# Optimization experiments

Hardware: AMD Instinct MI355X
Metric: run time of the kernel (lower is better)

## Reference

```python
import jax, jax.numpy as jnp
import numpy as np

K = 32  # kneighbors
BN_EPS = 1e-5


def setup_inputs() -> dict:
    key = jax.random.key(0)
    ks = jax.random.split(key, 8)
    B, N, S, C = 8, 4096, 1024, 64
    Cin = C + 6  # 70
    inp = {
        "xyz": jax.random.normal(ks[0], (B, N, 3), jnp.float32),
        "points": jax.random.normal(ks[1], (B, C, N), jnp.float32),
        "new_xyz": jax.random.normal(ks[2], (B, S, 3), jnp.float32),
        "W1": jax.random.normal(ks[3], (128, Cin), jnp.float32) / np.sqrt(Cin),
        "b1": jax.random.normal(ks[4], (128,), jnp.float32) * 0.01,
        "g1": jnp.ones((128,), jnp.float32),
        "be1": jnp.zeros((128,), jnp.float32),
        "W2": jax.random.normal(ks[5], (256, 128), jnp.float32) / np.sqrt(128),
        "b2": jax.random.normal(ks[6], (256,), jnp.float32) * 0.01,
        "g2": jnp.ones((256,), jnp.float32),
        "be2": jnp.zeros((256,), jnp.float32),
    }
    return inp


def _forward(xyz, points, new_xyz, W1, b1, g1, be1, W2, b2, g2, be2):
    B, S, _ = new_xyz.shape
    pts = jnp.transpose(points, (0, 2, 1))  # [B,N,C]
    # squared pairwise distances [B,S,N]
    sqd = (jnp.sum(new_xyz ** 2, -1)[:, :, None]
           + jnp.sum(xyz ** 2, -1)[:, None, :]
           - 2.0 * jnp.einsum('bsc,bnc->bsn', new_xyz, xyz))
    _, idx = jax.lax.top_k(-sqd, K)  # k smallest -> [B,S,K] int32
    gather = jax.vmap(lambda a, i: a[i])  # per-batch fancy gather
    gxyz = gather(xyz, idx)   # [B,S,K,3]
    gpts = gather(pts, idx)   # [B,S,K,C]
    q = jnp.broadcast_to(new_xyz[:, :, None, :], (B, S, K, 3))
    g = jnp.concatenate([gpts, gxyz, q], axis=-1)  # [B,S,K,C+6]
    x = jnp.transpose(g, (0, 3, 2, 1))  # [B,Cin,K,S]
    for W, b, gm, bt in ((W1, b1, g1, be1), (W2, b2, g2, be2)):
        x = jnp.einsum('oi,biks->boks', W, x) + b[None, :, None, None]
        mu = jnp.mean(x, axis=(0, 2, 3), keepdims=True)
        var = jnp.var(x, axis=(0, 2, 3), keepdims=True)  # biased, as torch BN train
        x = (x - mu) * jax.lax.rsqrt(var + BN_EPS)
        x = x * gm[None, :, None, None] + bt[None, :, None, None]
        x = jax.nn.relu(x)
    new_points = jnp.max(x, axis=2)  # [B,Cout,S]
    return new_xyz, new_points


def reference(xyz, points, new_xyz, W1, b1, g1, be1, W2, b2, g2, be2):
    return _forward(xyz, points, new_xyz, W1, b1, g1, be1, W2, b2, g2, be2)
```

## Files before the change

kernel.cpp:

```cpp
#include <hip/hip_runtime.h>
#include <stdint.h>

constexpr int Bn = 8, Nn = 4096, Sn = 1024, Cc = 64, KNN = 32, C1 = 128, C2 = 256;
constexpr int Qq = Bn * Sn;
constexpr int Mm = Qq * KNN;
constexpr int OUT_XYZ = Bn * Sn * 3;
constexpr float BNEPS = 1e-5f;
constexpr unsigned RSEL = 9;

constexpr size_t SZ_IDX  = (size_t)Qq * KNN * 4;
constexpr size_t SZ_PTST = (size_t)Bn * Nn * Cc * 2;
constexpr int    NB_MLP  = Mm / 64;
constexpr size_t SZ_P1   = (size_t)NB_MLP * 256 * 4;
constexpr size_t SZ_P2   = (size_t)NB_MLP * 512 * 4;
constexpr size_t OFF_IDX  = 0;
constexpr size_t OFF_PTST = OFF_IDX + SZ_IDX;
constexpr size_t OFF_P1   = OFF_PTST + SZ_PTST;
constexpr size_t OFF_P2   = OFF_P1 + SZ_P1;
constexpr size_t OFF_P1B  = OFF_P2 + SZ_P2;
constexpr size_t OFF_P2B  = OFF_P1B + (size_t)128 * 256 * 4;
constexpr size_t OFF_BN1  = OFF_P2B + (size_t)128 * 512 * 4;
constexpr size_t OFF_W2F  = OFF_BN1 + 1024;
constexpr size_t OFF_W1F  = OFF_W2F + (size_t)32768 * 2;
constexpr size_t OFF_VAL  = (OFF_W1F + (size_t)12288 * 2 + 255) & ~(size_t)255;

typedef __attribute__((ext_vector_type(8))) __bf16 bf16x8;
typedef __attribute__((ext_vector_type(4))) float f32x4;

__device__ __forceinline__ unsigned short f2bf(float f) {
  unsigned u = __float_as_uint(f);
  u = u + 0x7FFFu + ((u >> 16) & 1u);
  return (unsigned short)(u >> 16);
}

__device__ __forceinline__ void agg_hist(unsigned* hist, unsigned bin, bool valid, int lane) {
  bool todo = valid;
  while (true) {
    unsigned long long bm = __ballot(todo);
    if (bm == 0ull) break;
    int first = __ffsll(bm) - 1;
    unsigned b = (unsigned)__shfl((int)bin, first);
    unsigned long long m = __ballot(todo && bin == b);
    if (lane == first) atomicAdd(&hist[b], (unsigned)__popcll(m));
    if (todo && bin == b) todo = false;
  }
}

__global__ __launch_bounds__(256) void k_knn(const float* __restrict__ xyz,
                                             const float* __restrict__ nxyz,
                                             int* __restrict__ idxout,
                                             const float* __restrict__ pts,
                                             const float* __restrict__ W1,
                                             const float* __restrict__ W2,
                                             unsigned short* __restrict__ ptsTbf,
                                             float* __restrict__ outdst,
                                             unsigned short* __restrict__ w1f,
                                             unsigned short* __restrict__ w2f) {
  int t = threadIdx.x;
  if (blockIdx.x >= (unsigned)Qq) {
    int blk = blockIdx.x - Qq;
    if (blk < 512) {
      __shared__ float tile[64][65];
      int b = blk >> 6, n0 = (blk & 63) * 64;
      int cl = t & 63, rw = t >> 6;
#pragma unroll
      for (int i = 0; i < 16; ++i) {
        int c = i * 4 + rw;
        tile[cl][c] = pts[((size_t)b * Cc + c) * Nn + n0 + cl];
      }
      __syncthreads();
#pragma unroll
      for (int i = 0; i < 16; ++i) {
        int nf = i * 4 + rw;
        ptsTbf[((size_t)b * Nn + n0 + nf) * Cc + cl] = f2bf(tile[nf][cl]);
      }
    } else if (blk < 608) {
      int i = t + (blk - 512) * 256;
      if (i < OUT_XYZ) outdst[i] = nxyz[i];
    } else if (blk < 656) {
      int u = t + (blk - 608) * 256;
      int j = u & 7, lane = (u >> 3) & 63, rest = u >> 9;
      int ks = rest % 3, nt = rest / 3;
      int ch = nt * 16 + (lane & 15);
      int k = ks * 32 + (lane >> 4) * 8 + j;
      w1f[u] = (k < 70) ? f2bf(W1[ch * 70 + k]) : (unsigned short)0;
    } else {
      int u = t + (blk - 656) * 256;
      int j = u & 7, lane = (u >> 3) & 63, ks = (u >> 9) & 3, ntile = u >> 11;
      int col = ntile * 16 + (lane & 15);
      int k = ks * 32 + (lane >> 4) * 8 + j;
      w2f[u] = f2bf(W2[col * C1 + k]);
    }
    return;
  }
  int q = blockIdx.x, b = q >> 10;
  int lane = t & 63, w = t >> 6;
  const float4* xb4 = reinterpret_cast<const float4*>(xyz + (size_t)b * Nn * 3);
  float qx = nxyz[q * 3 + 0], qy = nxyz[q * 3 + 1], qz = nxyz[q * 3 + 2];
  unsigned key[16];
  {
#pragma clang fp contract(off)
    float sqq = (qx * qx + qy * qy) + qz * qz;
#pragma unroll
    for (int h = 0; h < 2; ++h) {
      float fl[24];
#pragma unroll
      for (int j = 0; j < 6; ++j) {
        float4 v = xb4[t * 12 + h * 6 + j];
        fl[4 * j + 0] = v.x; fl[4 * j + 1] = v.y; fl[4 * j + 2] = v.z; fl[4 * j + 3] = v.w;
      }
#pragma unroll
      for (int i = 0; i < 8; ++i) {
        float xl = fl[3 * i], yl = fl[3 * i + 1], zl = fl[3 * i + 2];
        float sqp = (xl * xl + yl * yl) + zl * zl;
        float dot = __builtin_fmaf(qz, zl, __builtin_fmaf(qy, yl, qx * xl));
        float d = (sqq + sqp) - 2.0f * dot;
        unsigned u = __float_as_uint(d);
        key[h * 8 + i] = (u & 0x80000000u) ? ~u : (u | 0x80000000u);
      }
    }
  }
  __shared__ unsigned long long buf64[256];
  __shared__ unsigned hist[256];
  __shared__ unsigned hist2[256];
  __shared__ unsigned wsum[4];
  __shared__ unsigned sel_bin, sel_off, cnt, ovf, thrU, tieflag;
  __shared__ unsigned eqcnt;
  __shared__ int eqbuf[128];

  unsigned s0 = key[0], s1 = key[8];
  hist[t] = 0;
  hist2[t] = 0;
  if (t == 0) { cnt = 0; ovf = 0; thrU = 0xFFFFFFFFu; tieflag = 0; }
  __syncthreads();
  agg_hist(hist, s0 >> 24, true, lane);
  agg_hist(hist, s1 >> 24, true, lane);
  __syncthreads();
  {
    unsigned h = hist[t], v = h;
#pragma unroll
    for (int off = 1; off < 64; off <<= 1) {
      unsigned o = __shfl_up(v, off);
      if (lane >= off) v += o;
    }
    if (lane == 63) wsum[w] = v;
    __syncthreads();
    unsigned woff = 0;
    for (int ww = 0; ww < w; ++ww) woff += wsum[ww];
    v += woff;
    unsigned vex = v - h;
    if (vex < RSEL && RSEL <= v) { sel_bin = (unsigned)t; sel_off = RSEL - vex; }
    __syncthreads();
  }
  unsigned sbin = sel_bin, srem = sel_off;
  if ((s0 >> 24) == sbin) atomicAdd(&hist2[(s0 >> 16) & 255u], 1u);
  if ((s1 >> 24) == sbin) atomicAdd(&hist2[(s1 >> 16) & 255u], 1u);
  __syncthreads();
  {
    unsigned h = hist2[t], v = h;
#pragma unroll
    for (int off = 1; off < 64; off <<= 1) {
      unsigned o = __shfl_up(v, off);
      if (lane >= off) v += o;
    }
    if (lane == 63) wsum[w] = v;
    __syncthreads();
    unsigned woff = 0;
    for (int ww = 0; ww < w; ++ww) woff += wsum[ww];
    v += woff;
    unsigned vex = v - h;
    if (vex < srem && srem <= v) {
      unsigned p16 = (sbin << 8) | (unsigned)t;
      thrU = (p16 >= 0xFFFFu) ? 0xFFFFFFFFu : ((p16 + 1u) << 16);
    }
    __syncthreads();
  }
  unsigned U = thrU;
#pragma unroll
  for (int i = 0; i < 16; ++i) {
    bool take = key[i] < U;
    unsigned long long m = __ballot(take);
    if (m == 0ull) continue;
    unsigned base = 0;
    if (lane == 0) base = atomicAdd(&cnt, (unsigned)__popcll(m));
    base = (unsigned)__shfl((int)base, 0);
    if (take) {
      unsigned off = base + (unsigned)__popcll(m & ((1ull << lane) - 1ull));
      if (off < 256u)
        buf64[off] = ((unsigned long long)key[i] << 32) | (unsigned)(t * 16 + i);
      else
        ovf = 1;
    }
  }
  __syncthreads();
  unsigned ncnt = cnt;
  if (!ovf && ncnt >= (unsigned)KNN && ncnt <= 256u) {
    int nc = (int)ncnt;
    const unsigned* keyhw = reinterpret_cast<const unsigned*>(buf64);
    int r = 0;
    bool own = false;
    int cid = 0;
    if (nc <= 64) {
      unsigned mykey = (lane < nc) ? keyhw[2 * lane + 1] : 0xFFFFFFFFu;
      int partial = 0;
      int base = w * 16;
#pragma unroll
      for (int ii = 0; ii < 16; ++ii) {
        int i = base + ii;
        bool inr = (i < nc);
        unsigned ok = (unsigned)__builtin_amdgcn_readlane((int)mykey, i);
        partial += (inr && ok < mykey);
      }
      hist[w * 64 + lane] = (unsigned)partial;
      __syncthreads();
      if (t < 64) {
        r = (int)(hist[t] + hist[64 + t] + hist[128 + t] + hist[192 + t]);
        cid = t;
        own = (t < nc);
      }
    } else if (nc <= 128) {
      cid = t & 127;
      bool haveC = (cid < nc);
      unsigned mykey = haveC ? keyhw[2 * cid + 1] : 0xFFFFFFFFu;
      int partial = 0;
      int c = t >> 7;
      if (c * 64 < nc) {
        int ci = c * 64 + lane;
        unsigned bk = (ci < nc) ? keyhw[2 * ci + 1] : 0xFFFFFFFFu;
#pragma unroll
        for (int i = 0; i < 64; ++i) {
          unsigned ok = (unsigned)__builtin_amdgcn_readlane((int)bk, i);
          partial += (ok < mykey);
        }
      }
      hist[t] = (unsigned)partial;
      __syncthreads();
      if (t < 128) {
        r = (int)(hist[t] + hist[t + 128]);
        own = haveC;
      }
    } else {
      cid = t;
      bool haveC = (t < nc);
      unsigned mykey = haveC ? keyhw[2 * t + 1] : 0xFFFFFFFFu;
      int nchunk = (nc + 63) >> 6;
      for (int c = 0; c < nchunk; ++c) {
        int ci = c * 64 + lane;
        unsigned bk = (ci < nc) ? keyhw[2 * ci + 1] : 0xFFFFFFFFu;
#pragma unroll
        for (int i = 0; i < 64; ++i) {
          unsigned ok = (unsigned)__builtin_amdgcn_readlane((int)bk, i);
          r += (ok < mykey);
        }
      }
      own = haveC;
    }
    hist2[t] = 0;
    __syncthreads();
    if (own) atomicAdd(&hist2[r], 1u);
    __syncthreads();
    if (hist2[t] > 1u) tieflag = 1;
    __syncthreads();
    if (tieflag) {
      bool own2 = (t < nc);
      unsigned long long my64 = own2 ? buf64[t] : ~0ull;
      int rr = 0;
      int nchunk = (nc + 63) >> 6;
      for (int c = 0; c < nchunk; ++c) {
        int ci = c * 64 + lane;
        unsigned long long v = (ci < nc) ? buf64[ci] : ~0ull;
        unsigned vlo = (unsigned)v, vhi = (unsigned)(v >> 32);
#pragma unroll
        for (int i = 0; i < 64; ++i) {
          unsigned olo = (unsigned)__builtin_amdgcn_readlane((int)vlo, i);
          unsigned ohi = (unsigned)__builtin_amdgcn_readlane((int)vhi, i);
          unsigned long long o = ((unsigned long long)ohi << 32) | olo;
          rr += (o < my64);
        }
      }
      if (own2 && rr < KNN) idxout[q * KNN + rr] = (int)keyhw[2 * t];
    } else {
      if (own && r < KNN) idxout[q * KNN + r] = (int)keyhw[2 * cid];
    }
  } else {
    unsigned prefix = 0, remaining = (unsigned)KNN;
    if (t == 0) { cnt = 0; eqcnt = 0; }
#pragma unroll
    for (int shift = 24; shift >= 0; shift -= 8) {
      hist[t] = 0;
      __syncthreads();
      unsigned himask = (shift == 24) ? 0u : (0xFFFFFFFFu << ((shift + 8) & 31));
#pragma unroll
      for (int i = 0; i < 16; ++i)
        if ((key[i] & himask) == prefix)
          atomicAdd(&hist[(key[i] >> shift) & 255], 1u);
      __syncthreads();
      unsigned h = hist[t], v = h;
#pragma unroll
      for (int off = 1; off < 64; off <<= 1) {
        unsigned o = __shfl_up(v, off);
        if (lane >= off) v += o;
      }
      if (lane == 63) wsum[w] = v;
      __syncthreads();
      unsigned woff = 0;
      for (int ww = 0; ww < w; ++ww) woff += wsum[ww];
      v += woff;
      unsigned vex = v - h;
      if (vex < remaining && remaining <= v) { sel_bin = (unsigned)t; sel_off = vex; }
      __syncthreads();
      prefix |= sel_bin << shift;
      remaining -= sel_off;
    }
#pragma unroll
    for (int i = 0; i < 16; ++i) {
      int p = t * 16 + i;
      if (key[i] < prefix) {
        unsigned pos = atomicAdd(&cnt, 1u);
        idxout[q * KNN + pos] = p;
      } else if (key[i] == prefix) {
        unsigned e = atomicAdd(&eqcnt, 1u);
        if (e < 128u) eqbuf[e] = p;
      }
    }
    __syncthreads();
    if (t == 0) {
      int n = (int)min(eqcnt, 128u);
      for (int a = 1; a < n; ++a) {
        int x = eqbuf[a], bi = a - 1;
        while (bi >= 0 && eqbuf[bi] > x) { eqbuf[bi + 1] = eqbuf[bi]; --bi; }
        eqbuf[bi + 1] = x;
      }
      int base = (int)cnt;
      for (int j = 0; j < (int)remaining; ++j) idxout[q * KNN + base + j] = eqbuf[j];
    }
  }
}

__device__ __forceinline__ void stage_gather(unsigned short* zs,
                                             const unsigned short* __restrict__ ptsTbf,
                                             const float* __restrict__ xyz,
                                             const float* __restrict__ nxyz,
                                             const int* __restrict__ idx,
                                             int m0, int b, int t) {
  int j = t >> 2, part = t & 3;
  int m = m0 + j;
  int pid = idx[m];
  const uint4* src =
      reinterpret_cast<const uint4*>(ptsTbf + ((size_t)b * Nn + pid) * Cc + part * 16);
  char* zc = reinterpret_cast<char*>(zs);
  int base = j * 256, swz = (j & 7) << 4;
  uint4 s0 = src[0], s1 = src[1];
  *reinterpret_cast<uint4*>(zc + ((base + part * 32) ^ swz)) = s0;
  *reinterpret_cast<uint4*>(zc + ((base + part * 32 + 16) ^ swz)) = s1;
  uint4 ex = make_uint4(0u, 0u, 0u, 0u);
  if (part == 0) {
    const float* xp = xyz + ((size_t)b * Nn + pid) * 3;
    int s = (m >> 5) & (Sn - 1);
    const float* qp = nxyz + (size_t)(b * Sn + s) * 3;
    ex.x = (unsigned)f2bf(xp[0]) | ((unsigned)f2bf(xp[1]) << 16);
    ex.y = (unsigned)f2bf(xp[2]) | ((unsigned)f2bf(qp[0]) << 16);
    ex.z = (unsigned)f2bf(qp[1]) | ((unsigned)f2bf(qp[2]) << 16);
  }
  *reinterpret_cast<uint4*>(zc + ((base + (8 + part) * 16) ^ swz)) = ex;
}

__global__ __launch_bounds__(256) void k_mlp1s(const unsigned short* __restrict__ ptsTbf,
                                               const float* __restrict__ xyz,
                                               const float* __restrict__ nxyz,
                                               const int* __restrict__ idx,
                                               const unsigned short* __restrict__ w1f,
                                               const float* __restrict__ b1,
                                               float* __restrict__ part1) {
  __shared__ unsigned short zs[64 * 128];
  int t = threadIdx.x;
  int m0 = blockIdx.x * 64;
  int b = m0 >> 15;
  int lane = t & 63, w = t >> 6;
  bf16x8 bfrag[2][3];
  {
    const uint4* wp = reinterpret_cast<const uint4*>(w1f);
#pragma unroll
    for (int nt = 0; nt < 2; ++nt)
#pragma unroll
      for (int ks = 0; ks < 3; ++ks)
        bfrag[nt][ks] = __builtin_bit_cast(bf16x8, wp[((w * 2 + nt) * 3 + ks) * 64 + lane]);
  }
  stage_gather(zs, ptsTbf, xyz, nxyz, idx, m0, b, t);
  __syncthreads();
  f32x4 acc[4][2];
#pragma unroll
  for (int mt = 0; mt < 4; ++mt)
#pragma unroll
    for (int nt = 0; nt < 2; ++nt) acc[mt][nt] = f32x4{0.f, 0.f, 0.f, 0.f};
  int r15 = lane & 15, rhi = lane >> 4;
  const char* zc = reinterpret_cast<const char*>(zs);
#pragma unroll
  for (int mt = 0; mt < 4; ++mt) {
    int row = mt * 16 + r15;
    bf16x8 af[3];
#pragma unroll
    for (int ks = 0; ks < 3; ++ks)
      af[ks] = __builtin_bit_cast(
          bf16x8, *reinterpret_cast<const uint4*>(
                      zc + ((row * 256 + ks * 64 + rhi * 16) ^ ((row & 7) << 4))));
#pragma unroll
    for (int nt = 0; nt < 2; ++nt)
#pragma unroll
      for (int ks = 0; ks < 3; ++ks)
        acc[mt][nt] =
            __builtin_amdgcn_mfma_f32_16x16x32_bf16(af[ks], bfrag[nt][ks], acc[mt][nt], 0, 0, 0);
  }
#pragma unroll
  for (int nt = 0; nt < 2; ++nt) {
    int col = w * 32 + nt * 16 + r15;
    float bv = b1[col];
    float s = 0.f, ss = 0.f;
#pragma unroll
    for (int mt = 0; mt < 4; ++mt)
#pragma unroll
      for (int rg = 0; rg < 4; ++rg) {
        float v = acc[mt][nt][rg] + bv;
        s += v; ss += v * v;
      }
    s += __shfl_xor(s, 16); s += __shfl_xor(s, 32);
    ss += __shfl_xor(ss, 16); ss += __shfl_xor(ss, 32);
    if (lane < 16) {
      part1[(size_t)blockIdx.x * 256 + col] = s;
      part1[(size_t)blockIdx.x * 256 + 128 + col] = ss;
    }
  }
}

__global__ __launch_bounds__(256) void k_red1a(const float* __restrict__ part1,
                                               float* __restrict__ p1b) {
  int t = threadIdx.x, r = blockIdx.x;
  float acc = 0.f;
  for (int row = r * 32; row < r * 32 + 32; ++row)
    acc += part1[(size_t)row * 256 + t];
  p1b[r * 256 + t] = acc;
}
__global__ __launch_bounds__(256) void k_red1b(const float* __restrict__ p1b,
                                               const float* __restrict__ b1,
                                               const float* __restrict__ g1,
                                               const float* __restrict__ be1,
                                               float* __restrict__ bn1) {
  __shared__ float lds[256];
  int t = threadIdx.x;
  float acc = 0.f;
  for (int row = 0; row < 128; ++row) acc += p1b[row * 256 + t];
  lds[t] = acc;
  __syncthreads();
  if (t < 128) {
    float sum = lds[t], ss = lds[128 + t];
    float mean = sum / (float)Mm;
    float var = ss / (float)Mm - mean * mean;
    float a = g1[t] * rsqrtf(var + BNEPS);
    bn1[t] = a;
    bn1[128 + t] = a * b1[t] + (be1[t] - mean * a);
  }
}

__global__ __launch_bounds__(256) void k_m2f(const unsigned short* __restrict__ ptsTbf,
                                             const float* __restrict__ xyz,
                                             const float* __restrict__ nxyz,
                                             const int* __restrict__ idx,
                                             const unsigned short* __restrict__ w1f,
                                             const float* __restrict__ bn1c,
                                             const unsigned short* __restrict__ w2f,
                                             const float* __restrict__ b2,
                                             const float* __restrict__ g2,
                                             float* __restrict__ part2,
                                             float* __restrict__ valv) {
  __shared__ unsigned short zs[64 * 128];
  __shared__ float bns[256];
  int t = threadIdx.x;
  int m0 = blockIdx.x * 64;
  int b = m0 >> 15;
  int lane = t & 63, w = t >> 6;
  bns[t] = bn1c[t];
  bf16x8 b1frag[2][3];
  {
    const uint4* wp = reinterpret_cast<const uint4*>(w1f);
#pragma unroll
    for (int nt = 0; nt < 2; ++nt)
#pragma unroll
      for (int ks = 0; ks < 3; ++ks)
        b1frag[nt][ks] = __builtin_bit_cast(bf16x8, wp[((w * 2 + nt) * 3 + ks) * 64 + lane]);
  }
  stage_gather(zs, ptsTbf, xyz, nxyz, idx, m0, b, t);
  __syncthreads();
  int r15 = lane & 15, rhi = lane >> 4;
  f32x4 acc1[4][2];
#pragma unroll
  for (int mt = 0; mt < 4; ++mt)
#pragma unroll
    for (int nt = 0; nt < 2; ++nt) acc1[mt][nt] = f32x4{0.f, 0.f, 0.f, 0.f};
  {
    const char* zc = reinterpret_cast<const char*>(zs);
#pragma unroll
    for (int mt = 0; mt < 4; ++mt) {
      int row = mt * 16 + r15;
      bf16x8 af[3];
#pragma unroll
      for (int ks = 0; ks < 3; ++ks)
        af[ks] = __builtin_bit_cast(
            bf16x8, *reinterpret_cast<const uint4*>(
                        zc + ((row * 256 + ks * 64 + rhi * 16) ^ ((row & 7) << 4))));
#pragma unroll
      for (int nt = 0; nt < 2; ++nt)
#pragma unroll
        for (int ks = 0; ks < 3; ++ks)
          acc1[mt][nt] = __builtin_amdgcn_mfma_f32_16x16x32_bf16(af[ks], b1frag[nt][ks],
                                                                 acc1[mt][nt], 0, 0, 0);
    }
  }
  __syncthreads();
  {
    char* zcw = reinterpret_cast<char*>(zs);
#pragma unroll
    for (int nt = 0; nt < 2; ++nt) {
      int col = w * 32 + nt * 16 + r15;
      float a = bns[col], c = bns[128 + col];
#pragma unroll
      for (int mt = 0; mt < 4; ++mt)
#pragma unroll
        for (int rg = 0; rg < 4; ++rg) {
          int row = mt * 16 + rhi * 4 + rg;
          float z = fmaxf(0.f, a * acc1[mt][nt][rg] + c);
          *reinterpret_cast<unsigned short*>(
              zcw + ((row * 256 + col * 2) ^ ((row & 7) << 4))) = f2bf(z);
        }
    }
  }
  __syncthreads();
  bf16x8 b2frag[4][4];
  {
    const uint4* wp = reinterpret_cast<const uint4*>(w2f) + (size_t)(w * 4) * 4 * 64 + lane;
#pragma unroll
    for (int nt = 0; nt < 4; ++nt)
#pragma unroll
      for (int ks = 0; ks < 4; ++ks)
        b2frag[nt][ks] = __builtin_bit_cast(bf16x8, wp[(nt * 4 + ks) * 64]);
  }
  f32x4 acc[4][4];
#pragma unroll
  for (int mt = 0; mt < 4; ++mt)
#pragma unroll
    for (int nt = 0; nt < 4; ++nt) acc[mt][nt] = f32x4{0.f, 0.f, 0.f, 0.f};
  {
    const char* zc = reinterpret_cast<const char*>(zs);
#pragma unroll
    for (int mt = 0; mt < 4; ++mt) {
      int row = mt * 16 + r15;
      bf16x8 af[4];
#pragma unroll
      for (int ks = 0; ks < 4; ++ks)
        af[ks] = __builtin_bit_cast(
            bf16x8, *reinterpret_cast<const uint4*>(
                        zc + ((row * 256 + ks * 64 + rhi * 16) ^ ((row & 7) << 4))));
#pragma unroll
      for (int nt = 0; nt < 4; ++nt)
#pragma unroll
        for (int ks = 0; ks < 4; ++ks)
          acc[mt][nt] = __builtin_amdgcn_mfma_f32_16x16x32_bf16(af[ks], b2frag[nt][ks],
                                                                acc[mt][nt], 0, 0, 0);
    }
  }
  int wn0 = w * 64;
  int q0 = m0 >> 5;
#pragma unroll
  for (int nt = 0; nt < 4; ++nt) {
    int col = wn0 + nt * 16 + r15;
    float bv = b2[col];
    bool pos = (g2[col] >= 0.0f);
    float s = 0.f, ss = 0.f;
    float mA = -3.0e38f, mB = -3.0e38f, nA = 3.0e38f, nB = 3.0e38f;
#pragma unroll
    for (int mt = 0; mt < 4; ++mt)
#pragma unroll
      for (int rg = 0; rg < 4; ++rg) {
        float v = acc[mt][nt][rg] + bv;
        s += v; ss += v * v;
        if (mt < 2) { mA = fmaxf(mA, v); nA = fminf(nA, v); }
        else        { mB = fmaxf(mB, v); nB = fminf(nB, v); }
      }
    float vA = pos ? mA : nA, vB = pos ? mB : nB;
    s += __shfl_xor(s, 16); s += __shfl_xor(s, 32);
    ss += __shfl_xor(ss, 16); ss += __shfl_xor(ss, 32);
    if (pos) {
      vA = fmaxf(vA, __shfl_xor(vA, 16)); vA = fmaxf(vA, __shfl_xor(vA, 32));
      vB = fmaxf(vB, __shfl_xor(vB, 16)); vB = fmaxf(vB, __shfl_xor(vB, 32));
    } else {
      vA = fminf(vA, __shfl_xor(vA, 16)); vA = fminf(vA, __shfl_xor(vA, 32));
      vB = fminf(vB, __shfl_xor(vB, 16)); vB = fminf(vB, __shfl_xor(vB, 32));
    }
    if (lane < 16) {
      part2[(size_t)blockIdx.x * 512 + col] = s;
      part2[(size_t)blockIdx.x * 512 + 256 + col] = ss;
    }
    if (lane < 32) {
      int q = q0 + (lane >> 4);
      valv[(size_t)q * C2 + col] = (lane < 16) ? vA : vB;
    }
  }
}

__global__ __launch_bounds__(512) void k_red2a(const float* __restrict__ part2,
                                               float* __restrict__ p2b) {
  int t = threadIdx.x, r = blockIdx.x;
  float acc = 0.f;
  for (int row = r * 32; row < r * 32 + 32; ++row)
    acc += part2[(size_t)row * 512 + t];
  p2b[r * 512 + t] = acc;
}

__global__ __launch_bounds__(256) void k_out(const float* __restrict__ valv,
                                             const float* __restrict__ p2b,
                                             const float* __restrict__ g2,
                                             const float* __restrict__ be2,
                                             float* __restrict__ out) {
  __shared__ float tile[64][65];
  __shared__ float sred[256], ssred[256];
  __shared__ float as_[64], cs_[64];
  int b = blockIdx.z, col0 = blockIdx.y * 64, s0 = blockIdx.x * 64;
  int t = threadIdx.x;
  int colL = t & 63, grp = t >> 6;
  {
    int col = col0 + colL;
    float s = 0.f, ss = 0.f;
    for (int row = grp * 32; row < grp * 32 + 32; ++row) {
      s += p2b[row * 512 + col];
      ss += p2b[row * 512 + 256 + col];
    }
    sred[grp * 64 + colL] = s;
    ssred[grp * 64 + colL] = ss;
  }
  __syncthreads();
  if (grp == 0) {
    float S = sred[colL] + sred[64 + colL] + sred[128 + colL] + sred[192 + colL];
    float SS = ssred[colL] + ssred[64 + colL] + ssred[128 + colL] + ssred[192 + colL];
    float mean = S / (float)Mm;
    float var = SS / (float)Mm - mean * mean;
    float a = g2[col0 + colL] * rsqrtf(var + BNEPS);
    as_[colL] = a;
    cs_[colL] = be2[col0 + colL] - mean * a;
  }
  __syncthreads();
  float a = as_[colL], c = cs_[colL];
  int sr = grp;
#pragma unroll
  for (int i = 0; i < 16; ++i) {
    int sl = sr * 16 + i;
    size_t q = (size_t)(b * Sn + s0 + sl);
    float v = valv[q * C2 + col0 + colL];
    tile[colL][sl] = fmaxf(0.f, a * v + c);
  }
  __syncthreads();
  int sl = t & 63, cr = t >> 6;
#pragma unroll
  for (int i = 0; i < 16; ++i) {
    int chl2 = i * 4 + cr;
    out[OUT_XYZ + ((size_t)(b * C2 + col0 + chl2)) * Sn + s0 + sl] = tile[chl2][sl];
  }
}

extern "C" void kernel_launch(void* const* d_in, const int* in_sizes, int n_in,
                              void* d_out, int out_size, void* d_ws, size_t ws_size,
                              hipStream_t stream) {
  (void)in_sizes; (void)n_in; (void)out_size; (void)ws_size;
  const float* xyz  = (const float*)d_in[0];
  const float* pts  = (const float*)d_in[1];
  const float* nxyz = (const float*)d_in[2];
  const float* W1   = (const float*)d_in[3];
  const float* b1   = (const float*)d_in[4];
  const float* g1   = (const float*)d_in[5];
  const float* be1  = (const float*)d_in[6];
  const float* W2   = (const float*)d_in[7];
  const float* b2   = (const float*)d_in[8];
  const float* g2   = (const float*)d_in[9];
  const float* be2  = (const float*)d_in[10];
  float* out = (float*)d_out;
  char* ws = (char*)d_ws;

  int*            idx    = (int*)(ws + OFF_IDX);
  unsigned short* ptsTbf = (unsigned short*)(ws + OFF_PTST);
  float*          part1  = (float*)(ws + OFF_P1);
  float*          part2  = (float*)(ws + OFF_P2);
  float*          p1b    = (float*)(ws + OFF_P1B);
  float*          p2b    = (float*)(ws + OFF_P2B);
  float*          bn1    = (float*)(ws + OFF_BN1);
  unsigned short* w2f    = (unsigned short*)(ws + OFF_W2F);
  unsigned short* w1f    = (unsigned short*)(ws + OFF_W1F);
  float*          valv   = (float*)(ws + OFF_VAL);

  k_knn<<<Qq + 784, 256, 0, stream>>>(xyz, nxyz, idx, pts, W1, W2, ptsTbf, out, w1f, w2f);
  k_mlp1s<<<NB_MLP, 256, 0, stream>>>(ptsTbf, xyz, nxyz, idx, w1f, b1, part1);
  k_red1a<<<128, 256, 0, stream>>>(part1, p1b);
  k_red1b<<<1, 256, 0, stream>>>(p1b, b1, g1, be1, bn1);
  k_m2f<<<NB_MLP, 256, 0, stream>>>(ptsTbf, xyz, nxyz, idx, w1f, bn1, w2f, b2, g2, part2, valv);
  k_red2a<<<128, 512, 0, stream>>>(part2, p2b);
  k_out<<<dim3(Sn / 64, C2 / 64, Bn), 256, 0, stream>>>(valv, p2b, g2, be2, out);
}
```

Baseline: 125.7 us.

## Use 128-row tiles in MLP1 stats kernel and simplify KNN rank ties

The first-layer statistics kernel now handles 128 gathered rows per block instead of 64, using a new staging routine where two threads load each row. This halves the block count and the partial-sum rows that the reduction reads, and reuses the weight fragments loaded into registers over more rows. Separately, the KNN rank step now always compares full 64-bit key+index values, so the tie-detection histogram pass and its extra barriers are gone. The larger tile doubles accumulator registers and LDS per block, which may lower occupancy. The small-candidate paths now do two readlanes per comparison.

```diff
diff --git a/kernel.cpp b/kernel.cpp
--- a/kernel.cpp
+++ b/kernel.cpp
@@ -11,7 +11,8 @@
 constexpr size_t SZ_IDX  = (size_t)Qq * KNN * 4;
 constexpr size_t SZ_PTST = (size_t)Bn * Nn * Cc * 2;
 constexpr int    NB_MLP  = Mm / 64;
-constexpr size_t SZ_P1   = (size_t)NB_MLP * 256 * 4;
+constexpr int    NB_M1   = Mm / 128;
+constexpr size_t SZ_P1   = (size_t)NB_M1 * 256 * 4;
 constexpr size_t SZ_P2   = (size_t)NB_MLP * 512 * 4;
 constexpr size_t OFF_IDX  = 0;
 constexpr size_t OFF_PTST = OFF_IDX + SZ_IDX;
@@ -124,14 +125,14 @@
   __shared__ unsigned hist[256];
   __shared__ unsigned hist2[256];
   __shared__ unsigned wsum[4];
-  __shared__ unsigned sel_bin, sel_off, cnt, ovf, thrU, tieflag;
+  __shared__ unsigned sel_bin, sel_off, cnt, ovf, thrU;
   __shared__ unsigned eqcnt;
   __shared__ int eqbuf[128];
 
   unsigned s0 = key[0], s1 = key[8];
   hist[t] = 0;
   hist2[t] = 0;
-  if (t == 0) { cnt = 0; ovf = 0; thrU = 0xFFFFFFFFu; tieflag = 0; }
+  if (t == 0) { cnt = 0; ovf = 0; thrU = 0xFFFFFFFFu; }
   __syncthreads();
   agg_hist(hist, s0 >> 24, true, lane);
   agg_hist(hist, s1 >> 24, true, lane);
@@ -196,75 +197,51 @@
   unsigned ncnt = cnt;
   if (!ovf && ncnt >= (unsigned)KNN && ncnt <= 256u) {
     int nc = (int)ncnt;
-    const unsigned* keyhw = reinterpret_cast<const unsigned*>(buf64);
-    int r = 0;
-    bool own = false;
-    int cid = 0;
     if (nc <= 64) {
-      unsigned mykey = (lane < nc) ? keyhw[2 * lane + 1] : 0xFFFFFFFFu;
+      unsigned long long my64 = (lane < nc) ? buf64[lane] : ~0ull;
+      unsigned mylo = (unsigned)my64, myhi = (unsigned)(my64 >> 32);
       int partial = 0;
       int base = w * 16;
 #pragma unroll
       for (int ii = 0; ii < 16; ++ii) {
         int i = base + ii;
-        bool inr = (i < nc);
-        unsigned ok = (unsigned)__builtin_amdgcn_readlane((int)mykey, i);
-        partial += (inr && ok < mykey);
-      }
-      hist[w * 64 + lane] = (unsigned)partial;
-      __syncthreads();
-      if (t < 64) {
-        r = (int)(hist[t] + hist[64 + t] + hist[128 + t] + hist[192 + t]);
-        cid = t;
-        own = (t < nc);
-      }
-    } else if (nc <= 128) {
-      cid = t & 127;
-      bool haveC = (cid < nc);
-      unsigned mykey = haveC ? keyhw[2 * cid + 1] : 0xFFFFFFFFu;
-      int partial = 0;
-      int c = t >> 7;
-      if (c * 64 < nc) {
-        int ci = c * 64 + lane;
-        unsigned bk = (ci < nc) ? keyhw[2 * ci + 1] : 0xFFFFFFFFu;
-#pragma unroll
-        for (int i = 0; i < 64; ++i) {
-          unsigned ok = (unsigned)__builtin_amdgcn_readlane((int)bk, i);
-          partial += (ok < mykey);
-        }
+        unsigned olo = (unsigned)__builtin_amdgcn_readlane((int)mylo, i);
+        unsigned ohi = (unsigned)__builtin_amdgcn_readlane((int)myhi, i);
+        unsigned long long o = ((unsigned long long)ohi << 32) | olo;
+        partial += (i < nc && o < my64);
       }
       hist[t] = (unsigned)partial;
       __syncthreads();
-      if (t < 128) {
-        r = (int)(hist[t] + hist[t + 128]);
-        own = haveC;
+      if (t < nc) {
+        int r = (int)(hist[t] + hist[64 + t] + hist[128 + t] + hist[192 + t]);
+        if (r < KNN) idxout[q * KNN + r] = (int)(unsigned)(buf64[t] & 0xFFFFFFFFull);
+      }
+    } else if (nc <= 128) {
+      int cid = t & 127;
+      unsigned long long my64 = (cid < nc) ? buf64[cid] : ~0ull;
+      int c = t >> 7;
+      int ci = c * 64 + lane;
+      unsigned long long ch64 = (ci < nc) ? buf64[ci] : ~0ull;
+      unsigned clo = (unsigned)ch64, chi = (unsigned)(ch64 >> 32);
+      int partial = 0;
+      if (c * 64 < nc) {
+#pragma unroll
+        for (int i = 0; i < 64; ++i) {
+          unsigned olo = (unsigned)__builtin_amdgcn_readlane((int)clo, i);
+          unsigned ohi = (unsigned)__builtin_amdgcn_readlane((int)chi, i);
+          unsigned long long o = ((unsigned long long)ohi << 32) | olo;
+          partial += (o < my64);
+        }
+      }
+      hist[t] = (unsigned)partial;
+      __syncthreads();
+      if (t < nc) {
+        int r = (int)(hist[t] + hist[t + 128]);
+        if (r < KNN) idxout[q * KNN + r] = (int)(unsigned)(buf64[t] & 0xFFFFFFFFull);
       }
     } else {
-      cid = t;
-      bool haveC = (t < nc);
-      unsigned mykey = haveC ? keyhw[2 * t + 1] : 0xFFFFFFFFu;
-      int nchunk = (nc + 63) >> 6;
-      for (int c = 0; c < nchunk; ++c) {
-        int ci = c * 64 + lane;
-        unsigned bk = (ci < nc) ? keyhw[2 * ci + 1] : 0xFFFFFFFFu;
-#pragma unroll
-        for (int i = 0; i < 64; ++i) {
-          unsigned ok = (unsigned)__builtin_amdgcn_readlane((int)bk, i);
-          r += (ok < mykey);
-        }
-      }
-      own = haveC;
-    }
-    hist2[t] = 0;
-    __syncthreads();
-    if (own) atomicAdd(&hist2[r], 1u);
-    __syncthreads();
-    if (hist2[t] > 1u) tieflag = 1;
-    __syncthreads();
-    if (tieflag) {
-      bool own2 = (t < nc);
-      unsigned long long my64 = own2 ? buf64[t] : ~0ull;
-      int rr = 0;
+      unsigned long long my64 = (t < nc) ? buf64[t] : ~0ull;
+      int r = 0;
       int nchunk = (nc + 63) >> 6;
       for (int c = 0; c < nchunk; ++c) {
         int ci = c * 64 + lane;
@@ -275,12 +252,10 @@
           unsigned olo = (unsigned)__builtin_amdgcn_readlane((int)vlo, i);
           unsigned ohi = (unsigned)__builtin_amdgcn_readlane((int)vhi, i);
           unsigned long long o = ((unsigned long long)ohi << 32) | olo;
-          rr += (o < my64);
+          r += (o < my64);
         }
       }
-      if (own2 && rr < KNN) idxout[q * KNN + rr] = (int)keyhw[2 * t];
-    } else {
-      if (own && r < KNN) idxout[q * KNN + r] = (int)keyhw[2 * cid];
+      if (t < nc && r < KNN) idxout[q * KNN + r] = (int)(unsigned)(buf64[t] & 0xFFFFFFFFull);
     }
   } else {
     unsigned prefix = 0, remaining = (unsigned)KNN;
@@ -365,6 +340,40 @@
   *reinterpret_cast<uint4*>(zc + ((base + (8 + part) * 16) ^ swz)) = ex;
 }
 
+__device__ __forceinline__ void stage_gather128(unsigned short* zs,
+                                                const unsigned short* __restrict__ ptsTbf,
+                                                const float* __restrict__ xyz,
+                                                const float* __restrict__ nxyz,
+                                                const int* __restrict__ idx,
+                                                int m0, int b, int t) {
+  int j = t >> 1, part = t & 1;
+  int m = m0 + j;
+  int pid = idx[m];
+  const uint4* src =
+      reinterpret_cast<const uint4*>(ptsTbf + ((size_t)b * Nn + pid) * Cc + part * 32);
+  char* zc = reinterpret_cast<char*>(zs);
+  int base = j * 256, swz = (j & 7) << 4;
+#pragma unroll
+  for (int u = 0; u < 4; ++u)
+    *reinterpret_cast<uint4*>(zc + ((base + part * 64 + u * 16) ^ swz)) = src[u];
+  if (part == 0) {
+    uint4 ex = make_uint4(0u, 0u, 0u, 0u);
+    const float* xp = xyz + ((size_t)b * Nn + pid) * 3;
+    int s = (m >> 5) & (Sn - 1);
+    const float* qp = nxyz + (size_t)(b * Sn + s) * 3;
+    ex.x = (unsigned)f2bf(xp[0]) | ((unsigned)f2bf(xp[1]) << 16);
+    ex.y = (unsigned)f2bf(xp[2]) | ((unsigned)f2bf(qp[0]) << 16);
+    ex.z = (unsigned)f2bf(qp[1]) | ((unsigned)f2bf(qp[2]) << 16);
+    *reinterpret_cast<uint4*>(zc + ((base + 128) ^ swz)) = ex;
+    uint4 z0 = make_uint4(0u, 0u, 0u, 0u);
+    *reinterpret_cast<uint4*>(zc + ((base + 144) ^ swz)) = z0;
+  } else {
+    uint4 z0 = make_uint4(0u, 0u, 0u, 0u);
+    *reinterpret_cast<uint4*>(zc + ((base + 160) ^ swz)) = z0;
+    *reinterpret_cast<uint4*>(zc + ((base + 176) ^ swz)) = z0;
+  }
+}
+
 __global__ __launch_bounds__(256) void k_mlp1s(const unsigned short* __restrict__ ptsTbf,
                                                const float* __restrict__ xyz,
                                                const float* __restrict__ nxyz,
@@ -372,9 +381,9 @@
                                                const unsigned short* __restrict__ w1f,
                                                const float* __restrict__ b1,
                                                float* __restrict__ part1) {
-  __shared__ unsigned short zs[64 * 128];
+  __shared__ unsigned short zs[128 * 128];
   int t = threadIdx.x;
-  int m0 = blockIdx.x * 64;
+  int m0 = blockIdx.x * 128;
   int b = m0 >> 15;
   int lane = t & 63, w = t >> 6;
   bf16x8 bfrag[2][3];
@@ -386,17 +395,17 @@
       for (int ks = 0; ks < 3; ++ks)
         bfrag[nt][ks] = __builtin_bit_cast(bf16x8, wp[((w * 2 + nt) * 3 + ks) * 64 + lane]);
   }
-  stage_gather(zs, ptsTbf, xyz, nxyz, idx, m0, b, t);
-  __syncthreads();
-  f32x4 acc[4][2];
-#pragma unroll
-  for (int mt = 0; mt < 4; ++mt)
+  stage_gather128(zs, ptsTbf, xyz, nxyz, idx, m0, b, t);
+  __syncthreads();
+  f32x4 acc[8][2];
+#pragma unroll
+  for (int mt = 0; mt < 8; ++mt)
 #pragma unroll
     for (int nt = 0; nt < 2; ++nt) acc[mt][nt] = f32x4{0.f, 0.f, 0.f, 0.f};
   int r15 = lane & 15, rhi = lane >> 4;
   const char* zc = reinterpret_cast<const char*>(zs);
 #pragma unroll
-  for (int mt = 0; mt < 4; ++mt) {
+  for (int mt = 0; mt < 8; ++mt) {
     int row = mt * 16 + r15;
     bf16x8 af[3];
 #pragma unroll
@@ -417,7 +426,7 @@
     float bv = b1[col];
     float s = 0.f, ss = 0.f;
 #pragma unroll
-    for (int mt = 0; mt < 4; ++mt)
+    for (int mt = 0; mt < 8; ++mt)
 #pragma unroll
       for (int rg = 0; rg < 4; ++rg) {
         float v = acc[mt][nt][rg] + bv;
@@ -436,7 +445,7 @@
                                                float* __restrict__ p1b) {
   int t = threadIdx.x, r = blockIdx.x;
   float acc = 0.f;
-  for (int row = r * 32; row < r * 32 + 32; ++row)
+  for (int row = r * 16; row < r * 16 + 16; ++row)
     acc += part1[(size_t)row * 256 + t];
   p1b[r * 256 + t] = acc;
 }
@@ -695,7 +704,7 @@
   float*          valv   = (float*)(ws + OFF_VAL);
 
   k_knn<<<Qq + 784, 256, 0, stream>>>(xyz, nxyz, idx, pts, W1, W2, ptsTbf, out, w1f, w2f);
-  k_mlp1s<<<NB_MLP, 256, 0, stream>>>(ptsTbf, xyz, nxyz, idx, w1f, b1, part1);
+  k_mlp1s<<<NB_M1, 256, 0, stream>>>(ptsTbf, xyz, nxyz, idx, w1f, b1, part1);
   k_red1a<<<128, 256, 0, stream>>>(part1, p1b);
   k_red1b<<<1, 256, 0, stream>>>(p1b, b1, g1, be1, bn1);
   k_m2f<<<NB_MLP, 256, 0, stream>>>(ptsTbf, xyz, nxyz, idx, w1f, bn1, w2f, b2, g2, part2, valv);
```

After: 127.2 us. About the same (+1.2%).
